# Kernel optimization log

Measured on AMD Instinct MI355X. Metric: run time of the kernel, lower is better.

The kernel has to match this reference:

```python
import jax, jax.numpy as jnp
import numpy as np

B, S, IN, OUT = 4, 32, 8192, 8192


def setup_inputs() -> dict:
    key = jax.random.key(0)
    k1, k2, k3, k4 = jax.random.split(key, 4)
    x = jax.random.normal(k1, (B, S, IN), dtype=jnp.float32)
    # FP8-e4m3 stored weight: round-trip through fp8 so values are representable,
    # then keep as fp32 (the module upcasts to fp32 before the matmul anyway).
    w = jax.random.normal(k2, (OUT, IN), dtype=jnp.float32)
    weight = w.astype(jnp.float8_e4m3fn).astype(jnp.float32)
    # per-output-channel scale, strictly positive small values
    weight_scale = jax.random.uniform(k3, (OUT, 1), dtype=jnp.float32,
                                      minval=1e-3, maxval=2e-2)
    bias = (jax.random.normal(k4, (OUT,), dtype=jnp.float32) * 0.01).astype(jnp.float16)
    return {"x": x, "weight": weight, "weight_scale": weight_scale, "bias": bias}


def reference(x, weight, weight_scale, bias):
    # dequantize fp8 weight to fp32 with per-channel scale  [OUT, IN]
    dq_w = weight * weight_scale
    # x @ dq_w.T  -> [B, S, OUT]
    out = jnp.einsum("bsi,oi->bso", x.astype(jnp.float32), dq_w)
    out = out + bias.astype(jnp.float32)
    return out
```

## Files before the change

### kernel.cpp

```cpp
#include <hip/hip_runtime.h>
#include <hip/hip_bf16.h>
#include <hip/hip_fp16.h>


namespace {
constexpr int NN = 8192;
constexpr int KK = 8192;
constexpr int KSPLIT = 4;
constexpr int KPB = KK / KSPLIT;
constexpr int BKT = 512;
constexpr int NIT = KPB / BKT;

constexpr size_t XOFF = 0;
constexpr size_t POFF = (size_t)128 * KK * 2;
constexpr size_t PSZ  = (size_t)128 * NN * 4;
constexpr size_t WS_NEED = POFF + (size_t)KSPLIT * PSZ;

typedef __attribute__((ext_vector_type(8))) short bf16x8;
typedef __attribute__((ext_vector_type(4))) float f32x4;

__device__ __forceinline__ bf16x8 pack8(float4 a, float4 b) {
    union { __hip_bfloat16 h[8]; bf16x8 v; } p;
    p.h[0] = __float2bfloat16(a.x); p.h[1] = __float2bfloat16(a.y);
    p.h[2] = __float2bfloat16(a.z); p.h[3] = __float2bfloat16(a.w);
    p.h[4] = __float2bfloat16(b.x); p.h[5] = __float2bfloat16(b.y);
    p.h[6] = __float2bfloat16(b.z); p.h[7] = __float2bfloat16(b.w);
    return p.v;
}

__device__ __forceinline__ void gload_lds16(const void* g, void* l) {
    __builtin_amdgcn_global_load_lds(
        (const __attribute__((address_space(1))) unsigned int*)g,
        (__attribute__((address_space(3))) unsigned int*)l,
        16, 0, 0);
}
}

#define RAW_BARRIER() asm volatile("s_barrier" ::: "memory")
#define VMWAIT(N_)    asm volatile("s_waitcnt vmcnt(" #N_ ")" ::: "memory")

__global__ __launch_bounds__(256)
void cfp8_xprep(const float* __restrict__ x, unsigned char* __restrict__ ws)
{
    const int g = blockIdx.x * 256 + threadIdx.x;
    const float4* src = (const float4*)x + (size_t)g * 2;
    float4 a = src[0], b = src[1];
    const int m  = g >> 10;
    const int kg = g & 1023;
    const int s  = kg >> 2;
    const int r8 = kg & 3;
    const int t  = m >> 4;
    const int lm = m & 15;
    const int l  = r8 * 16 + lm;
    union { __hip_bfloat16 h[8]; uint4 u; } p;
    p.h[0] = __float2bfloat16(a.x); p.h[1] = __float2bfloat16(a.y);
    p.h[2] = __float2bfloat16(a.z); p.h[3] = __float2bfloat16(a.w);
    p.h[4] = __float2bfloat16(b.x); p.h[5] = __float2bfloat16(b.y);
    p.h[6] = __float2bfloat16(b.z); p.h[7] = __float2bfloat16(b.w);
    ((uint4*)(ws + XOFF))[(size_t)(s * 8 + t) * 64 + l] = p.u;
}

__global__ __launch_bounds__(256, 4)
void cfp8_gemm_r15(const float* __restrict__ w, const unsigned char* __restrict__ ws,
                   float* __restrict__ part)
{
    __shared__ __align__(16) __hip_bfloat16 lw[32 * BKT];

    const int tid  = threadIdx.x;
    const int lane = tid & 63;
    const int wid  = tid >> 6;
    const int l16  = lane & 15;
    const int quad = lane >> 4;
    const int bid  = blockIdx.x;
    const int kz   = bid & 3;
    const int n0   = (bid >> 2) * 32;
    const size_t kbase = (size_t)kz * KPB;

    const uint4* xr = (const uint4*)(ws + XOFF);

    f32x4 acc[2][2];
#pragma unroll
    for (int i = 0; i < 2; ++i)
#pragma unroll
        for (int j = 0; j < 2; ++j) acc[i][j] = (f32x4){0.f, 0.f, 0.f, 0.f};

    for (int c = 0; c < NIT; ++c) {
        if (c) __syncthreads();

#pragma unroll 1
        for (int rg = 0; rg < 2; ++rg) {
            float4 v[4][2];
#pragma unroll
            for (int rr = 0; rr < 4; ++rr) {
                const int r = wid * 8 + rg * 4 + rr;
                const float* src = w + (size_t)(n0 + r) * KK + kbase + c * BKT;
                v[rr][0] = *(const float4*)(src + lane * 4);
                v[rr][1] = *(const float4*)(src + 256 + lane * 4);
            }
#pragma unroll
            for (int rr = 0; rr < 4; ++rr) {
                const int r = wid * 8 + rg * 4 + rr;
#pragma unroll
                for (int i = 0; i < 2; ++i) {
                    const int g = i * 32 + (lane >> 1);
                    union { __hip_bfloat16 h[4]; uint2 u; } p;
                    p.h[0] = __float2bfloat16(v[rr][i].x);
                    p.h[1] = __float2bfloat16(v[rr][i].y);
                    p.h[2] = __float2bfloat16(v[rr][i].z);
                    p.h[3] = __float2bfloat16(v[rr][i].w);
                    *(uint2*)((char*)lw + r * 1024 +
                              ((g ^ (r & 7)) << 4) + (lane & 1) * 8) = p.u;
                }
            }
        }
        __syncthreads();

        const int ksg0 = kz * 64 + c * 16;
#pragma unroll 4
        for (int ks = 0; ks < 16; ++ks) {
            bf16x8 af[2], bf[2];
#pragma unroll
            for (int i = 0; i < 2; ++i) {
                uint4 u = xr[(size_t)((ksg0 + ks) * 8 + wid * 2 + i) * 64 + lane];
                af[i] = *(bf16x8*)&u;
            }
#pragma unroll
            for (int j = 0; j < 2; ++j) {
                const int row_ = j * 16 + l16;
                const int kc   = ks * 4 + quad;
                bf[j] = *(const bf16x8*)((const char*)lw + row_ * 1024 +
                                         ((kc ^ (row_ & 7)) << 4));
            }
#pragma unroll
            for (int i = 0; i < 2; ++i)
#pragma unroll
                for (int j = 0; j < 2; ++j)
                    acc[i][j] = __builtin_amdgcn_mfma_f32_16x16x32_bf16(
                        af[i], bf[j], acc[i][j], 0, 0, 0);
        }
    }

    float* pk = part + (size_t)kz * (PSZ / 4);
#pragma unroll
    for (int j = 0; j < 2; ++j) {
        const int col = n0 + j * 16 + l16;
#pragma unroll
        for (int i = 0; i < 2; ++i) {
            const int mb = wid * 32 + i * 16 + quad * 4;
#pragma unroll
            for (int r = 0; r < 4; ++r)
                pk[(size_t)(mb + r) * NN + col] = acc[i][j][r];
        }
    }
}

__global__ __launch_bounds__(256)
void cfp8_reduce(const float* __restrict__ part,
                 const float* __restrict__ c1, const float* __restrict__ c2,
                 float* __restrict__ out)
{
    __shared__ int s_c1s, s_kind;
    const int tid = threadIdx.x;
    if (tid < 64) {
        float v = c1[tid * 64];
        unsigned long long b = __ballot((v > 1e-4f) && (v < 0.5f));
        int c1s = (b == ~0ull) ? 1 : 0;
        const void* bp = c1s ? (const void*)c2 : (const void*)c1;
        float vf = __half2float(((const __half*)bp)[tid * 64]);
        unsigned long long bf_ = __ballot((vf < 0.5f) && (vf > -0.5f));
        float vb = __bfloat162float(((const __hip_bfloat16*)bp)[tid * 64]);
        unsigned long long bb = __ballot((vb < 0.5f) && (vb > -0.5f));
        if (tid == 0) {
            s_c1s  = c1s;
            s_kind = (bf_ == ~0ull) ? 0 : ((bb == ~0ull) ? 1 : 2);
        }
    }
    __syncthreads();

    const int g = blockIdx.x * 256 + tid;
    const float4* p4 = (const float4*)part;
    float4 s = p4[g];
#pragma unroll
    for (int kz = 1; kz < KSPLIT; ++kz) {
        float4 p = p4[(size_t)kz * (PSZ / 16) + g];
        s.x += p.x; s.y += p.y; s.z += p.z; s.w += p.w;
    }

    const int n = (g & 2047) * 4;
    const float* scalep = s_c1s ? c1 : c2;
    const void*  biasp  = s_c1s ? (const void*)c2 : (const void*)c1;
    float4 sc = *(const float4*)(scalep + n);
    float bs[4];
#pragma unroll
    for (int r = 0; r < 4; ++r) {
        if (s_kind == 0)      bs[r] = __half2float(((const __half*)biasp)[n + r]);
        else if (s_kind == 1) bs[r] = __bfloat162float(((const __hip_bfloat16*)biasp)[n + r]);
        else                  bs[r] = ((const float*)biasp)[n + r];
    }
    float4 o;
    o.x = s.x * sc.x + bs[0];
    o.y = s.y * sc.y + bs[1];
    o.z = s.z * sc.z + bs[2];
    o.w = s.w * sc.w + bs[3];
    ((float4*)out)[g] = o;
}

__global__ __launch_bounds__(256, 1)
void cfp8_gemm_r12(const float* __restrict__ x, const float* __restrict__ w,
                   const float* __restrict__ c1, const float* __restrict__ c2,
                   float* __restrict__ out)
{
    constexpr int BKF = 32;
    constexpr int NITF = KPB / BKF;
    __shared__ __align__(16) float ldsA[4][128 * BKF];
    __shared__ __align__(16) float ldsB[4][128 * BKF];
    __shared__ int s_c1s, s_kind;

    const int tid  = threadIdx.x;
    const int lane = tid & 63;
    const int wid  = tid >> 6;
    const int l16  = lane & 15;
    const int quad = lane >> 4;
    const int wr   = wid >> 1;
    const int wc   = wid & 1;
    const int bid  = blockIdx.x;
    const int kz   = bid & 3;
    const int nb0  = (bid >> 2) * 128;
    const size_t kbase = (size_t)kz * KPB;

    if (tid < 64) {
        float v = c1[tid * 64];
        unsigned long long b = __ballot((v > 1e-4f) && (v < 0.5f));
        int c1s = (b == ~0ull) ? 1 : 0;
        const void* bp = c1s ? (const void*)c2 : (const void*)c1;
        float vf = __half2float(((const __half*)bp)[tid * 64]);
        unsigned long long bf_ = __ballot((vf < 0.5f) && (vf > -0.5f));
        float vb = __bfloat162float(((const __hip_bfloat16*)bp)[tid * 64]);
        unsigned long long bb = __ballot((vb < 0.5f) && (vb > -0.5f));
        if (tid == 0) {
            s_c1s = c1s;
            s_kind = (bf_ == ~0ull) ? 0 : ((bb == ~0ull) ? 1 : 2);
        }
    }
    __syncthreads();

    unsigned off[4];
#pragma unroll
    for (int j = 0; j < 4; ++j) {
        const int q   = (wid * 4 + j) * 64 + lane;
        const int row = q >> 3;
        const int c8  = q & 7;
        const int swz = c8 ^ (row & 7);
        off[j] = (unsigned)row * (KK * 4) + (unsigned)swz * 16;
    }
    const char* xsrc = (const char*)(x + kbase);
    const char* wsrc = (const char*)(w + (size_t)nb0 * KK + kbase);

#define STAGE(slot_, c_)                                                       \
    {                                                                          \
        const size_t kb_ = (size_t)(c_) * (BKF * 4);                           \
        _Pragma("unroll")                                                      \
        for (int j = 0; j < 4; ++j) {                                          \
            gload_lds16(xsrc + kb_ + off[j],                                   \
                        (char*)&ldsA[slot_][0] + (wid * 4 + j) * 1024);        \
            gload_lds16(wsrc + kb_ + off[j],                                   \
                        (char*)&ldsB[slot_][0] + (wid * 4 + j) * 1024);        \
        }                                                                      \
    }
#define LOADFRAG(dst_, base_, rb_)                                             \
    {                                                                          \
        const int row_ = (rb_) + l16;                                          \
        const int sw_  = row_ & 7;                                             \
        float4 a0_ = *(const float4*)&(base_)[(row_ * 8 + ((quad * 2) ^ sw_)) * 4];     \
        float4 a1_ = *(const float4*)&(base_)[(row_ * 8 + ((quad * 2 + 1) ^ sw_)) * 4]; \
        dst_ = pack8(a0_, a1_);                                                \
    }
#define COMPUTE(slot_)                                                         \
    {                                                                          \
        const float* la_ = &ldsA[slot_][0];                                    \
        const float* lb_ = &ldsB[slot_][0];                                    \
        bf16x8 af_[4], bf_[4];                                                 \
        _Pragma("unroll")                                                      \
        for (int i = 0; i < 4; ++i) LOADFRAG(af_[i], la_, wr * 64 + i * 16)    \
        _Pragma("unroll")                                                      \
        for (int j = 0; j < 4; ++j) LOADFRAG(bf_[j], lb_, wc * 64 + j * 16)    \
        _Pragma("unroll")                                                      \
        for (int i = 0; i < 4; ++i)                                            \
            _Pragma("unroll")                                                  \
            for (int j = 0; j < 4; ++j)                                        \
                acc[i][j] = __builtin_amdgcn_mfma_f32_16x16x32_bf16(           \
                    af_[i], bf_[j], acc[i][j], 0, 0, 0);                       \
    }

    f32x4 acc[4][4];
#pragma unroll
    for (int i = 0; i < 4; ++i)
#pragma unroll
        for (int j = 0; j < 4; ++j) acc[i][j] = (f32x4){0.f, 0.f, 0.f, 0.f};

    STAGE(0, 0)
    STAGE(1, 1)
    STAGE(2, 2)
    for (int c = 0; c < NITF - 3; ++c) {
        VMWAIT(16);
        RAW_BARRIER();
        STAGE((c + 3) & 3, c + 3)
        COMPUTE(c & 3)
    }
    VMWAIT(16); RAW_BARRIER(); COMPUTE((NITF - 3) & 3)
    VMWAIT(8);  RAW_BARRIER(); COMPUTE((NITF - 2) & 3)
    VMWAIT(0);  RAW_BARRIER(); COMPUTE((NITF - 1) & 3)
#undef STAGE
#undef LOADFRAG
#undef COMPUTE

    const float* scalep = s_c1s ? c1 : c2;
    const void*  biasp  = s_c1s ? (const void*)c2 : (const void*)c1;
#pragma unroll
    for (int j = 0; j < 4; ++j) {
        const int col = nb0 + wc * 64 + j * 16 + l16;
        const float scj = scalep[col];
        float bsj = 0.0f;
        if (kz == 0) {
            if (s_kind == 0)      bsj = __half2float(((const __half*)biasp)[col]);
            else if (s_kind == 1) bsj = __bfloat162float(((const __hip_bfloat16*)biasp)[col]);
            else                  bsj = ((const float*)biasp)[col];
        }
#pragma unroll
        for (int i = 0; i < 4; ++i) {
            const int rb = wr * 64 + i * 16 + quad * 4;
#pragma unroll
            for (int r = 0; r < 4; ++r)
                atomicAdd(out + (size_t)(rb + r) * NN + col,
                          acc[i][j][r] * scj + bsj);
        }
    }
}

extern "C" void kernel_launch(void* const* d_in, const int* in_sizes, int n_in,
                              void* d_out, int out_size, void* d_ws, size_t ws_size,
                              hipStream_t stream) {
    int iw = 0;
    for (int i = 1; i < n_in; ++i) if (in_sizes[i] > in_sizes[iw]) iw = i;
    int ix = -1;
    for (int i = 0; i < n_in; ++i)
        if (i != iw && (ix < 0 || in_sizes[i] > in_sizes[ix])) ix = i;
    const float* c1 = nullptr;
    const float* c2 = nullptr;
    for (int i = 0; i < n_in; ++i) {
        if (i == iw || i == ix) continue;
        if (!c1) c1 = (const float*)d_in[i];
        else     c2 = (const float*)d_in[i];
    }
    const float* w = (const float*)d_in[iw];
    const float* x = (const float*)d_in[ix];
    float* out = (float*)d_out;

    if (d_ws != nullptr && ws_size >= WS_NEED) {
        unsigned char* ws = (unsigned char*)d_ws;
        float* part = (float*)(ws + POFF);
        cfp8_xprep<<<dim3(512), dim3(256), 0, stream>>>(x, ws);
        cfp8_gemm_r15<<<dim3(256 * KSPLIT), dim3(256), 0, stream>>>(w, ws, part);
        cfp8_reduce<<<dim3(1024), dim3(256), 0, stream>>>(part, c1, c2, out);
    } else {
        hipMemsetAsync(d_out, 0, (size_t)out_size * sizeof(float), stream);
        cfp8_gemm_r12<<<dim3(64 * KSPLIT), dim3(256), 0, stream>>>(x, w, c1, c2, out);
    }
}
```

Baseline: 383.8 us.

## Shrink N tile to 16 rows and stage full K-slice of weights once

Each block now handles 16 output columns instead of 32 and loads its whole 2048-wide K slice of weights into shared memory (64KB) in one pass, removing the inner chunk loop and its repeated barriers. The grid doubles to 2048 blocks and launch bounds drop to 2 blocks per CU. In exchange, activation fragments are reused across only one B fragment per step, so x traffic from L2 doubles. There is also no overlap between the weight load phase and the MFMA phase within a block.

```diff
diff --git a/kernel.cpp b/kernel.cpp
--- a/kernel.cpp
+++ b/kernel.cpp
@@ -8,8 +8,8 @@
 constexpr int KK = 8192;
 constexpr int KSPLIT = 4;
 constexpr int KPB = KK / KSPLIT;
-constexpr int BKT = 512;
-constexpr int NIT = KPB / BKT;
+constexpr int NR  = 16;
+constexpr int NKS = KPB / 32;
 
 constexpr size_t XOFF = 0;
 constexpr size_t POFF = (size_t)128 * KK * 2;
@@ -60,11 +60,11 @@
     ((uint4*)(ws + XOFF))[(size_t)(s * 8 + t) * 64 + l] = p.u;
 }
 
-__global__ __launch_bounds__(256, 4)
-void cfp8_gemm_r15(const float* __restrict__ w, const unsigned char* __restrict__ ws,
+__global__ __launch_bounds__(256, 2)
+void cfp8_gemm_r16(const float* __restrict__ w, const unsigned char* __restrict__ ws,
                    float* __restrict__ part)
 {
-    __shared__ __align__(16) __hip_bfloat16 lw[32 * BKT];
+    __shared__ __align__(16) __hip_bfloat16 lw[NR * KPB];
 
     const int tid  = threadIdx.x;
     const int lane = tid & 63;
@@ -73,84 +73,62 @@
     const int quad = lane >> 4;
     const int bid  = blockIdx.x;
     const int kz   = bid & 3;
-    const int n0   = (bid >> 2) * 32;
+    const int n0   = (bid >> 2) * NR;
     const size_t kbase = (size_t)kz * KPB;
 
     const uint4* xr = (const uint4*)(ws + XOFF);
 
-    f32x4 acc[2][2];
-#pragma unroll
-    for (int i = 0; i < 2; ++i)
-#pragma unroll
-        for (int j = 0; j < 2; ++j) acc[i][j] = (f32x4){0.f, 0.f, 0.f, 0.f};
-
-    for (int c = 0; c < NIT; ++c) {
-        if (c) __syncthreads();
-
 #pragma unroll 1
-        for (int rg = 0; rg < 2; ++rg) {
-            float4 v[4][2];
-#pragma unroll
-            for (int rr = 0; rr < 4; ++rr) {
-                const int r = wid * 8 + rg * 4 + rr;
-                const float* src = w + (size_t)(n0 + r) * KK + kbase + c * BKT;
-                v[rr][0] = *(const float4*)(src + lane * 4);
-                v[rr][1] = *(const float4*)(src + 256 + lane * 4);
-            }
-#pragma unroll
-            for (int rr = 0; rr < 4; ++rr) {
-                const int r = wid * 8 + rg * 4 + rr;
-#pragma unroll
-                for (int i = 0; i < 2; ++i) {
-                    const int g = i * 32 + (lane >> 1);
-                    union { __hip_bfloat16 h[4]; uint2 u; } p;
-                    p.h[0] = __float2bfloat16(v[rr][i].x);
-                    p.h[1] = __float2bfloat16(v[rr][i].y);
-                    p.h[2] = __float2bfloat16(v[rr][i].z);
-                    p.h[3] = __float2bfloat16(v[rr][i].w);
-                    *(uint2*)((char*)lw + r * 1024 +
-                              ((g ^ (r & 7)) << 4) + (lane & 1) * 8) = p.u;
-                }
-            }
-        }
-        __syncthreads();
-
-        const int ksg0 = kz * 64 + c * 16;
+    for (int rr = 0; rr < 4; ++rr) {
+        const int r = wid * 4 + rr;
+        const float* src = w + (size_t)(n0 + r) * KK + kbase;
+        float4 v[8];
+#pragma unroll
+        for (int i = 0; i < 8; ++i)
+            v[i] = *(const float4*)(src + i * 256 + lane * 4);
+#pragma unroll
+        for (int i = 0; i < 8; ++i) {
+            const int g = i * 32 + (lane >> 1);
+            union { __hip_bfloat16 h[4]; uint2 u; } p;
+            p.h[0] = __float2bfloat16(v[i].x);
+            p.h[1] = __float2bfloat16(v[i].y);
+            p.h[2] = __float2bfloat16(v[i].z);
+            p.h[3] = __float2bfloat16(v[i].w);
+            *(uint2*)((char*)lw + r * 4096 +
+                      ((g ^ (r & 7)) << 4) + (lane & 1) * 8) = p.u;
+        }
+    }
+    __syncthreads();
+
+    f32x4 acc[2];
+#pragma unroll
+    for (int i = 0; i < 2; ++i) acc[i] = (f32x4){0.f, 0.f, 0.f, 0.f};
+
 #pragma unroll 4
-        for (int ks = 0; ks < 16; ++ks) {
-            bf16x8 af[2], bf[2];
-#pragma unroll
-            for (int i = 0; i < 2; ++i) {
-                uint4 u = xr[(size_t)((ksg0 + ks) * 8 + wid * 2 + i) * 64 + lane];
-                af[i] = *(bf16x8*)&u;
-            }
-#pragma unroll
-            for (int j = 0; j < 2; ++j) {
-                const int row_ = j * 16 + l16;
-                const int kc   = ks * 4 + quad;
-                bf[j] = *(const bf16x8*)((const char*)lw + row_ * 1024 +
-                                         ((kc ^ (row_ & 7)) << 4));
-            }
-#pragma unroll
-            for (int i = 0; i < 2; ++i)
-#pragma unroll
-                for (int j = 0; j < 2; ++j)
-                    acc[i][j] = __builtin_amdgcn_mfma_f32_16x16x32_bf16(
-                        af[i], bf[j], acc[i][j], 0, 0, 0);
-        }
+    for (int ks = 0; ks < NKS; ++ks) {
+        const int ksg = kz * NKS + ks;
+        bf16x8 af[2];
+#pragma unroll
+        for (int i = 0; i < 2; ++i) {
+            uint4 u = xr[(size_t)(ksg * 8 + wid * 2 + i) * 64 + lane];
+            af[i] = *(bf16x8*)&u;
+        }
+        const int kc = ks * 4 + quad;
+        bf16x8 bf = *(const bf16x8*)((const char*)lw + l16 * 4096 +
+                                     ((kc ^ (l16 & 7)) << 4));
+#pragma unroll
+        for (int i = 0; i < 2; ++i)
+            acc[i] = __builtin_amdgcn_mfma_f32_16x16x32_bf16(af[i], bf, acc[i], 0, 0, 0);
     }
 
     float* pk = part + (size_t)kz * (PSZ / 4);
-#pragma unroll
-    for (int j = 0; j < 2; ++j) {
-        const int col = n0 + j * 16 + l16;
-#pragma unroll
-        for (int i = 0; i < 2; ++i) {
-            const int mb = wid * 32 + i * 16 + quad * 4;
-#pragma unroll
-            for (int r = 0; r < 4; ++r)
-                pk[(size_t)(mb + r) * NN + col] = acc[i][j][r];
-        }
+    const int col = n0 + l16;
+#pragma unroll
+    for (int i = 0; i < 2; ++i) {
+        const int mb = wid * 32 + i * 16 + quad * 4;
+#pragma unroll
+        for (int r = 0; r < 4; ++r)
+            pk[(size_t)(mb + r) * NN + col] = acc[i][r];
     }
 }
 
@@ -360,7 +338,7 @@
         unsigned char* ws = (unsigned char*)d_ws;
         float* part = (float*)(ws + POFF);
         cfp8_xprep<<<dim3(512), dim3(256), 0, stream>>>(x, ws);
-        cfp8_gemm_r15<<<dim3(256 * KSPLIT), dim3(256), 0, stream>>>(w, ws, part);
+        cfp8_gemm_r16<<<dim3((NN / NR) * KSPLIT), dim3(256), 0, stream>>>(w, ws, part);
         cfp8_reduce<<<dim3(1024), dim3(256), 0, stream>>>(part, c1, c2, out);
     } else {
         hipMemsetAsync(d_out, 0, (size_t)out_size * sizeof(float), stream);
```

After: 402.2 us. 1.05x slower.
